# Kernel optimization log

Hardware: AMD Instinct MI355X
Metric: run time of the kernel (lower is better)

Reference implementation:

```python
import jax, jax.numpy as jnp
import numpy as np


def setup_inputs() -> dict:
    key = jax.random.key(0)
    ks = jax.random.split(key, 6)
    B, d, S = 256, 512, 196  # batch, hidden dim, spatial locations (14x14)
    return {
        "memory_state": jax.random.normal(ks[0], (B, d), dtype=jnp.float32),
        "ctrl_state": jax.random.normal(ks[1], (B, d), dtype=jnp.float32),
        "kb_proj": jax.random.normal(ks[2], (B, d, S), dtype=jnp.float32),
        "W_concat": jax.random.normal(ks[3], (d, d), dtype=jnp.float32) * (1.0 / np.sqrt(d)),
        "b_concat": jax.random.normal(ks[4], (d,), dtype=jnp.float32) * 0.01,
        "w_attn": jax.random.normal(ks[5], (d,), dtype=jnp.float32) * (1.0 / np.sqrt(d)),
    }


def reference(memory_state, ctrl_state, kb_proj, W_concat, b_concat, w_attn):
    # I_elements: [B, S, d] -- elementwise gating of knowledge base by memory
    I_t = memory_state[:, :, None] * kb_proj           # [B, d, S]
    I_t = jnp.transpose(I_t, (0, 2, 1))                # [B, S, d]
    # concat_layer (torch Linear: x @ W^T + b) + residual with kb_proj
    concat = jnp.einsum('bsd,ed->bse', I_t, W_concat) + b_concat
    concat = concat + jnp.transpose(kb_proj, (0, 2, 1))  # [B, S, d]
    # attention logits: (concat * ctrl) @ w_attn -> [B, S]
    rai = jnp.einsum('bsd,d->bs', concat * ctrl_state[:, None, :], w_attn)
    rvi = jax.nn.softmax(rai, axis=1)                  # [B, S]
    # attention-weighted sum over spatial locations -> [B, d]
    read_vector = jnp.einsum('bs,bds->bd', rvi, kb_proj)
    return read_vector
```

## Files before the change

### kernel.cpp

```cpp
#include <hip/hip_runtime.h>
#include <math.h>

#define B 256
#define D 512
#define S 196

__global__ __launch_bounds__(512) void k_prep(const float* __restrict__ mem,
                                              const float* __restrict__ ctrl,
                                              const float* __restrict__ W,
                                              const float* __restrict__ w_attn,
                                              float* __restrict__ p) {
    __shared__ float u_s[D];
    const int b = blockIdx.x;
    const int t = threadIdx.x;
    float u = ctrl[b * D + t] * w_attn[t];
    u_s[t] = u;
    __syncthreads();
    float acc = 0.f;
#pragma unroll 8
    for (int e = 0; e < D; ++e) {
        acc += u_s[e] * W[e * D + t];
    }
    p[b * D + t] = mem[b * D + t] * acc + u;
}

__global__ __launch_bounds__(256) void k_attn(const float* __restrict__ kb,
                                              float* __restrict__ p_and_out) {
    __shared__ float p_s[D];
    __shared__ float rvi[S];
    __shared__ float red[8];
    const int b = blockIdx.x;
    const int t = threadIdx.x;
    const int lane = t & 63;
    const int wave = t >> 6;

    p_s[t]       = p_and_out[b * D + t];
    p_s[t + 256] = p_and_out[b * D + t + 256];
    __syncthreads();

    const float* kbb = kb + (size_t)b * D * S;

    float rai = -INFINITY;
    if (t < S) {
        float a0 = 0.f, a1 = 0.f, a2 = 0.f, a3 = 0.f;
#pragma unroll 4
        for (int d = 0; d < D; d += 4) {
            a0 += p_s[d + 0] * kbb[(d + 0) * S + t];
            a1 += p_s[d + 1] * kbb[(d + 1) * S + t];
            a2 += p_s[d + 2] * kbb[(d + 2) * S + t];
            a3 += p_s[d + 3] * kbb[(d + 3) * S + t];
        }
        rai = (a0 + a1) + (a2 + a3);
    }

    float m = rai;
#pragma unroll
    for (int o = 1; o < 64; o <<= 1) m = fmaxf(m, __shfl_xor(m, o, 64));
    if (lane == 0) red[wave] = m;
    __syncthreads();
    m = fmaxf(fmaxf(red[0], red[1]), fmaxf(red[2], red[3]));

    float ex = (t < S) ? __expf(rai - m) : 0.f;
    float sum = ex;
#pragma unroll
    for (int o = 1; o < 64; o <<= 1) sum += __shfl_xor(sum, o, 64);
    if (lane == 0) red[4 + wave] = sum;
    __syncthreads();
    const float l = red[4] + red[5] + red[6] + red[7];
    if (t < S) rvi[t] = ex / l;
    __syncthreads();

#pragma unroll
    for (int r = 0; r < 2; ++r) {
        const int e = t + r * 256;
        const float4* row = (const float4*)(kbb + (size_t)e * S);
        float acc = 0.f;
#pragma unroll 7
        for (int i = 0; i < S / 4; ++i) {
            float4 v = row[i];
            acc += rvi[4 * i + 0] * v.x + rvi[4 * i + 1] * v.y +
                   rvi[4 * i + 2] * v.z + rvi[4 * i + 3] * v.w;
        }
        p_and_out[b * D + e] = acc;
    }
}

extern "C" void kernel_launch(void* const* d_in, const int* in_sizes, int n_in,
                              void* d_out, int out_size, void* d_ws, size_t ws_size,
                              hipStream_t stream) {
    const float* mem  = (const float*)d_in[0];
    const float* ctrl = (const float*)d_in[1];
    const float* kb   = (const float*)d_in[2];
    const float* W    = (const float*)d_in[3];
    const float* wat  = (const float*)d_in[5];
    float* out = (float*)d_out;

    k_prep<<<B, D, 0, stream>>>(mem, ctrl, W, wat, out);
    k_attn<<<B, 256, 0, stream>>>(kb, out);
}
```

Baseline: 211.2 us.

## Split attention kernel into logits, softmax, weighted-sum stages with wider parallelism

Replaces the single per-batch attention kernel, which ran 256 blocks, with three kernels. The first computes partial logits over 8 row chunks per batch using float4 loads. The second reduces the partials and applies softmax. The third computes the weighted sum with one wavefront per output row. k_prep now processes 4 batches per block, so each W load is reused across batches. The intent is more blocks to raise occupancy and memory parallelism on kb, at the cost of reading kb twice across separate launches, extra workspace traffic and two more launches.

```diff
diff --git a/kernel.cpp b/kernel.cpp
--- a/kernel.cpp
+++ b/kernel.cpp
@@ -4,62 +4,91 @@
 #define B 256
 #define D 512
 #define S 196
+#define NCH 8
+#define ROWS_PER_CH (D / NCH)
+#define NPART 32
 
-__global__ __launch_bounds__(512) void k_prep(const float* __restrict__ mem,
+__global__ __launch_bounds__(256) void k_prep(const float* __restrict__ mem,
                                               const float* __restrict__ ctrl,
                                               const float* __restrict__ W,
                                               const float* __restrict__ w_attn,
                                               float* __restrict__ p) {
-    __shared__ float u_s[D];
-    const int b = blockIdx.x;
-    const int t = threadIdx.x;
-    float u = ctrl[b * D + t] * w_attn[t];
-    u_s[t] = u;
+    __shared__ float u_s[4][D];
+    const int bg   = blockIdx.x >> 1;
+    const int half = blockIdx.x & 1;
+    const int t    = threadIdx.x;
+    const int d    = half * 256 + t;
+    const int b0   = bg * 4;
+#pragma unroll
+    for (int i = 0; i < 8; ++i) {
+        int idx = i * 256 + t;
+        int j = idx >> 9, e = idx & 511;
+        u_s[j][e] = ctrl[(b0 + j) * D + e] * w_attn[e];
+    }
     __syncthreads();
-    float acc = 0.f;
+    float a0 = 0.f, a1 = 0.f, a2 = 0.f, a3 = 0.f;
 #pragma unroll 8
     for (int e = 0; e < D; ++e) {
-        acc += u_s[e] * W[e * D + t];
+        float wv = W[e * D + d];
+        a0 += u_s[0][e] * wv;
+        a1 += u_s[1][e] * wv;
+        a2 += u_s[2][e] * wv;
+        a3 += u_s[3][e] * wv;
     }
-    p[b * D + t] = mem[b * D + t] * acc + u;
+    p[(b0 + 0) * D + d] = mem[(b0 + 0) * D + d] * a0 + u_s[0][d];
+    p[(b0 + 1) * D + d] = mem[(b0 + 1) * D + d] * a1 + u_s[1][d];
+    p[(b0 + 2) * D + d] = mem[(b0 + 2) * D + d] * a2 + u_s[2][d];
+    p[(b0 + 3) * D + d] = mem[(b0 + 3) * D + d] * a3 + u_s[3][d];
 }
 
-__global__ __launch_bounds__(256) void k_attn(const float* __restrict__ kb,
-                                              float* __restrict__ p_and_out) {
-    __shared__ float p_s[D];
-    __shared__ float rvi[S];
+__global__ __launch_bounds__(256) void k_logits(const float* __restrict__ kb,
+                                                const float* __restrict__ p,
+                                                float* __restrict__ rai_part) {
+    __shared__ float p_s[ROWS_PER_CH];
+    const int bid = blockIdx.x;
+    const int b = bid >> 3, c = bid & 7;
+    const int t = threadIdx.x;
+    const int w = t >> 6, l = t & 63;
+    const int d0 = c * ROWS_PER_CH;
+    if (t < ROWS_PER_CH) p_s[t] = p[b * D + d0 + t];
+    __syncthreads();
+
+    const float* kbb = kb + (size_t)b * D * S + (size_t)d0 * S;
+    float4 acc = make_float4(0.f, 0.f, 0.f, 0.f);
+    if (l < 49) {
+#pragma unroll
+        for (int r = 0; r < 16; ++r) {
+            const int row = w * 16 + r;
+            const float4 v = *(const float4*)(kbb + row * S + l * 4);
+            const float pv = p_s[row];
+            acc.x += pv * v.x; acc.y += pv * v.y;
+            acc.z += pv * v.z; acc.w += pv * v.w;
+        }
+        float4* dst = (float4*)(rai_part + ((size_t)b * NPART + c * 4 + w) * S);
+        dst[l] = acc;
+    }
+}
+
+__global__ __launch_bounds__(256) void k_softmax(const float* __restrict__ rai_part,
+                                                 float* __restrict__ rvi) {
     __shared__ float red[8];
     const int b = blockIdx.x;
     const int t = threadIdx.x;
-    const int lane = t & 63;
-    const int wave = t >> 6;
-
-    p_s[t]       = p_and_out[b * D + t];
-    p_s[t + 256] = p_and_out[b * D + t + 256];
-    __syncthreads();
-
-    const float* kbb = kb + (size_t)b * D * S;
-
+    const int lane = t & 63, wave = t >> 6;
     float rai = -INFINITY;
     if (t < S) {
-        float a0 = 0.f, a1 = 0.f, a2 = 0.f, a3 = 0.f;
-#pragma unroll 4
-        for (int d = 0; d < D; d += 4) {
-            a0 += p_s[d + 0] * kbb[(d + 0) * S + t];
-            a1 += p_s[d + 1] * kbb[(d + 1) * S + t];
-            a2 += p_s[d + 2] * kbb[(d + 2) * S + t];
-            a3 += p_s[d + 3] * kbb[(d + 3) * S + t];
-        }
-        rai = (a0 + a1) + (a2 + a3);
+        float v = 0.f;
+        const float* src = rai_part + (size_t)b * NPART * S + t;
+#pragma unroll
+        for (int k = 0; k < NPART; ++k) v += src[k * S];
+        rai = v;
     }
-
     float m = rai;
 #pragma unroll
     for (int o = 1; o < 64; o <<= 1) m = fmaxf(m, __shfl_xor(m, o, 64));
     if (lane == 0) red[wave] = m;
     __syncthreads();
     m = fmaxf(fmaxf(red[0], red[1]), fmaxf(red[2], red[3]));
-
     float ex = (t < S) ? __expf(rai - m) : 0.f;
     float sum = ex;
 #pragma unroll
@@ -67,22 +96,29 @@
     if (lane == 0) red[4 + wave] = sum;
     __syncthreads();
     const float l = red[4] + red[5] + red[6] + red[7];
-    if (t < S) rvi[t] = ex / l;
+    if (t < S) rvi[b * S + t] = ex / l;
+}
+
+__global__ __launch_bounds__(256) void k_wsum(const float* __restrict__ kb,
+                                              const float* __restrict__ rvi,
+                                              float* __restrict__ out) {
+    __shared__ float rvi_s[S];
+    const int t = threadIdx.x;
+    const int w = t >> 6, l = t & 63;
+    const int R0 = blockIdx.x * 4;
+    const int b = R0 >> 9;
+    if (t < S) rvi_s[t] = rvi[b * S + t];
     __syncthreads();
-
+    const int e = (R0 & 511) + w;
+    float acc = 0.f;
+    if (l < 49) {
+        const float4 v = *(const float4*)(kb + ((size_t)b * D + e) * S + l * 4);
+        acc = rvi_s[4 * l + 0] * v.x + rvi_s[4 * l + 1] * v.y +
+              rvi_s[4 * l + 2] * v.z + rvi_s[4 * l + 3] * v.w;
+    }
 #pragma unroll
-    for (int r = 0; r < 2; ++r) {
-        const int e = t + r * 256;
-        const float4* row = (const float4*)(kbb + (size_t)e * S);
-        float acc = 0.f;
-#pragma unroll 7
-        for (int i = 0; i < S / 4; ++i) {
-            float4 v = row[i];
-            acc += rvi[4 * i + 0] * v.x + rvi[4 * i + 1] * v.y +
-                   rvi[4 * i + 2] * v.z + rvi[4 * i + 3] * v.w;
-        }
-        p_and_out[b * D + e] = acc;
-    }
+    for (int o = 1; o < 64; o <<= 1) acc += __shfl_xor(acc, o, 64);
+    if (l == 0) out[(size_t)b * D + e] = acc;
 }
 
 extern "C" void kernel_launch(void* const* d_in, const int* in_sizes, int n_in,
@@ -95,6 +131,11 @@
     const float* wat  = (const float*)d_in[5];
     float* out = (float*)d_out;
 
-    k_prep<<<B, D, 0, stream>>>(mem, ctrl, W, wat, out);
-    k_attn<<<B, 256, 0, stream>>>(kb, out);
+    float* rai_part = (float*)d_ws;
+    float* rvi      = rai_part + (size_t)B * NPART * S;
+
+    k_prep   <<<128,          256, 0, stream>>>(mem, ctrl, W, wat, out);
+    k_logits <<<B * NCH,      256, 0, stream>>>(kb, out, rai_part);
+    k_softmax<<<B,            256, 0, stream>>>(rai_part, rvi);
+    k_wsum   <<<B * D / 4,    256, 0, stream>>>(kb, rvi, out);
 }
```

New measurement: 376.2 us. 1.78x slower.

## Batch W reuse across four rows in prep and split attention rows across waves

Applied to the files above, without the earlier changes.

k_prep now handles four batch rows per block with float4 loads of W, so each W element is reused four times and fewer blocks stream the full matrix. The attention kernel uses 512 threads; each wave covers a 64-row slice of d and reads kb rows as contiguous float4, and partial logits are combined through shared memory. The read-vector pass keeps the same row layout and sums each row with a wave shuffle reduction. The intermediate now goes to the workspace buffer instead of the output, which adds shuffle-reduction work in exchange for wider, coalesced kb accesses.

```diff
diff --git a/kernel.cpp b/kernel.cpp
--- a/kernel.cpp
+++ b/kernel.cpp
@@ -4,84 +4,123 @@
 #define B 256
 #define D 512
 #define S 196
+#define SQ 49
 
 __global__ __launch_bounds__(512) void k_prep(const float* __restrict__ mem,
                                               const float* __restrict__ ctrl,
                                               const float* __restrict__ W,
                                               const float* __restrict__ w_attn,
                                               float* __restrict__ p) {
-    __shared__ float u_s[D];
+    __shared__ float u_s[4][D];
+    __shared__ float4 pp[4][4][128];
+    const int t = threadIdx.x;
+    const int b0 = blockIdx.x * 4;
+#pragma unroll
+    for (int i = 0; i < 4; ++i) {
+        int idx = i * 512 + t;
+        int j = idx >> 9, e = idx & 511;
+        u_s[j][e] = ctrl[(b0 + j) * D + e] * w_attn[e];
+    }
+    __syncthreads();
+    const int q = t & 127, c = t >> 7;
+    const float4* W4 = (const float4*)W;
+    float4 a0 = {0,0,0,0}, a1 = {0,0,0,0}, a2 = {0,0,0,0}, a3 = {0,0,0,0};
+#pragma unroll 8
+    for (int i = 0; i < 128; ++i) {
+        const int e = c * 128 + i;
+        const float4 wv = W4[e * 128 + q];
+        const float u0 = u_s[0][e], u1 = u_s[1][e], u2 = u_s[2][e], u3 = u_s[3][e];
+        a0.x += u0 * wv.x; a0.y += u0 * wv.y; a0.z += u0 * wv.z; a0.w += u0 * wv.w;
+        a1.x += u1 * wv.x; a1.y += u1 * wv.y; a1.z += u1 * wv.z; a1.w += u1 * wv.w;
+        a2.x += u2 * wv.x; a2.y += u2 * wv.y; a2.z += u2 * wv.z; a2.w += u2 * wv.w;
+        a3.x += u3 * wv.x; a3.y += u3 * wv.y; a3.z += u3 * wv.z; a3.w += u3 * wv.w;
+    }
+    pp[c][0][q] = a0; pp[c][1][q] = a1; pp[c][2][q] = a2; pp[c][3][q] = a3;
+    __syncthreads();
+    if (t < 128) {
+#pragma unroll
+        for (int j = 0; j < 4; ++j) {
+            float4 s0 = pp[0][j][t], s1 = pp[1][j][t], s2 = pp[2][j][t], s3 = pp[3][j][t];
+            float4 sm = {s0.x + s1.x + s2.x + s3.x, s0.y + s1.y + s2.y + s3.y,
+                         s0.z + s1.z + s2.z + s3.z, s0.w + s1.w + s2.w + s3.w};
+            const float4 m4 = ((const float4*)mem)[(b0 + j) * 128 + t];
+            const float4 u4 = ((const float4*)&u_s[j][0])[t];
+            float4 o;
+            o.x = m4.x * sm.x + u4.x; o.y = m4.y * sm.y + u4.y;
+            o.z = m4.z * sm.z + u4.z; o.w = m4.w * sm.w + u4.w;
+            ((float4*)p)[(b0 + j) * 128 + t] = o;
+        }
+    }
+}
+
+__global__ __launch_bounds__(512) void k_fused(const float* __restrict__ kb,
+                                               const float* __restrict__ p,
+                                               float* __restrict__ out) {
+    __shared__ float p_s[D];
+    __shared__ float part[8 * S];
+    __shared__ float rvi_s[S];
+    __shared__ float redm[8], reds[8];
     const int b = blockIdx.x;
     const int t = threadIdx.x;
-    float u = ctrl[b * D + t] * w_attn[t];
-    u_s[t] = u;
+    const int w = t >> 6, l = t & 63;
+    p_s[t] = p[b * D + t];
     __syncthreads();
-    float acc = 0.f;
+    const float* kbb = kb + (size_t)b * D * S;
+
+    float4 acc = {0.f, 0.f, 0.f, 0.f};
+    if (l < SQ) {
 #pragma unroll 8
-    for (int e = 0; e < D; ++e) {
-        acc += u_s[e] * W[e * D + t];
+        for (int k = 0; k < 64; ++k) {
+            const int row = w * 64 + k;
+            const float4 v = *(const float4*)(kbb + (size_t)row * S + 4 * l);
+            const float pv = p_s[row];
+            acc.x += pv * v.x; acc.y += pv * v.y;
+            acc.z += pv * v.z; acc.w += pv * v.w;
+        }
+        *(float4*)&part[w * S + 4 * l] = acc;
     }
-    p[b * D + t] = mem[b * D + t] * acc + u;
-}
-
-__global__ __launch_bounds__(256) void k_attn(const float* __restrict__ kb,
-                                              float* __restrict__ p_and_out) {
-    __shared__ float p_s[D];
-    __shared__ float rvi[S];
-    __shared__ float red[8];
-    const int b = blockIdx.x;
-    const int t = threadIdx.x;
-    const int lane = t & 63;
-    const int wave = t >> 6;
-
-    p_s[t]       = p_and_out[b * D + t];
-    p_s[t + 256] = p_and_out[b * D + t + 256];
     __syncthreads();
-
-    const float* kbb = kb + (size_t)b * D * S;
 
     float rai = -INFINITY;
     if (t < S) {
-        float a0 = 0.f, a1 = 0.f, a2 = 0.f, a3 = 0.f;
-#pragma unroll 4
-        for (int d = 0; d < D; d += 4) {
-            a0 += p_s[d + 0] * kbb[(d + 0) * S + t];
-            a1 += p_s[d + 1] * kbb[(d + 1) * S + t];
-            a2 += p_s[d + 2] * kbb[(d + 2) * S + t];
-            a3 += p_s[d + 3] * kbb[(d + 3) * S + t];
-        }
-        rai = (a0 + a1) + (a2 + a3);
+        float v = 0.f;
+#pragma unroll
+        for (int ww = 0; ww < 8; ++ww) v += part[ww * S + t];
+        rai = v;
     }
-
     float m = rai;
 #pragma unroll
     for (int o = 1; o < 64; o <<= 1) m = fmaxf(m, __shfl_xor(m, o, 64));
-    if (lane == 0) red[wave] = m;
+    if (l == 0) redm[w] = m;
     __syncthreads();
-    m = fmaxf(fmaxf(red[0], red[1]), fmaxf(red[2], red[3]));
-
+    m = redm[0];
+#pragma unroll
+    for (int ww = 1; ww < 8; ++ww) m = fmaxf(m, redm[ww]);
     float ex = (t < S) ? __expf(rai - m) : 0.f;
-    float sum = ex;
+    float sm = ex;
 #pragma unroll
-    for (int o = 1; o < 64; o <<= 1) sum += __shfl_xor(sum, o, 64);
-    if (lane == 0) red[4 + wave] = sum;
+    for (int o = 1; o < 64; o <<= 1) sm += __shfl_xor(sm, o, 64);
+    if (l == 0) reds[w] = sm;
     __syncthreads();
-    const float l = red[4] + red[5] + red[6] + red[7];
-    if (t < S) rvi[t] = ex / l;
+    float li = 0.f;
+#pragma unroll
+    for (int ww = 0; ww < 8; ++ww) li += reds[ww];
+    if (t < S) rvi_s[t] = ex / li;
     __syncthreads();
 
+    float4 rv = {0.f, 0.f, 0.f, 0.f};
+    if (l < SQ) rv = *(const float4*)&rvi_s[4 * l];
+#pragma unroll 4
+    for (int k = 0; k < 64; ++k) {
+        const int e = w * 64 + k;
+        float a = 0.f;
+        if (l < SQ) {
+            const float4 v = *(const float4*)(kbb + (size_t)e * S + 4 * l);
+            a = rv.x * v.x + rv.y * v.y + rv.z * v.z + rv.w * v.w;
+        }
 #pragma unroll
-    for (int r = 0; r < 2; ++r) {
-        const int e = t + r * 256;
-        const float4* row = (const float4*)(kbb + (size_t)e * S);
-        float acc = 0.f;
-#pragma unroll 7
-        for (int i = 0; i < S / 4; ++i) {
-            float4 v = row[i];
-            acc += rvi[4 * i + 0] * v.x + rvi[4 * i + 1] * v.y +
-                   rvi[4 * i + 2] * v.z + rvi[4 * i + 3] * v.w;
-        }
-        p_and_out[b * D + e] = acc;
+        for (int o = 1; o < 64; o <<= 1) a += __shfl_xor(a, o, 64);
+        if (l == 0) out[b * D + e] = a;
     }
 }
 
@@ -94,7 +133,8 @@
     const float* W    = (const float*)d_in[3];
     const float* wat  = (const float*)d_in[5];
     float* out = (float*)d_out;
+    float* pbuf = (float*)d_ws;
 
-    k_prep<<<B, D, 0, stream>>>(mem, ctrl, W, wat, out);
-    k_attn<<<B, 256, 0, stream>>>(kb, out);
+    k_prep <<<B / 4, 512, 0, stream>>>(mem, ctrl, W, wat, pbuf);
+    k_fused<<<B,     512, 0, stream>>>(kb, pbuf, out);
 }
```

After: 247.4 us. 17.2% more time.
